# Kernel tuning notes

Measured on AMD Instinct MI355X. Metric: run time of the kernel, lower is better.

## Reference

```python
import jax, jax.numpy as jnp
import numpy as np

SR = 16000
FLOOR = 60.0
EPS = 1e-12

# ---------- numpy helpers replicating the torch control flow (plan building) ----------

def _hann(n):
    # torch.hann_window default periodic=True: 0.5 - 0.5*cos(2*pi*k/n)
    if n <= 0:
        return np.zeros((0,), np.float32)
    return (0.5 - 0.5 * np.cos(2.0 * np.pi * np.arange(n) / n)).astype(np.float32)


def _interp_linear(p, T):
    # torch F.interpolate(mode='linear', align_corners=False) on [1,1,S] -> [1,1,T]
    S = p.shape[0]
    pos = (np.arange(T, dtype=np.float64) + 0.5) * (S / T) - 0.5
    pos = np.clip(pos, 0.0, S - 1)
    lo = np.floor(pos).astype(np.int64)
    hi = np.minimum(lo + 1, S - 1)
    frac = pos - lo
    return (p[lo] * (1.0 - frac) + p[hi] * frac).astype(np.float32)


def _find_voiced(f0, i):
    sub = f0[i:]
    if sub.size == 0:
        return None
    flag = (sub > 0.0).astype(np.int64)
    flag[0] = 0
    if not flag.any():
        return None
    idx = int(flag.argmax())
    rest = flag[idx:]
    z = np.nonzero(rest == 0)[0]
    cnt = int(z[0]) if z.size else int(rest.size)
    left = i + idx
    return left, left + cnt


def _find_allpeaks(sig, f0, sr, floor=FLOOR):
    T = sig.shape[0]
    gpeak = float(np.abs(sig).max())

    def find_peak(i, dir_):
        w = int(sr / max(float(f0[i]), floor))
        s = max(i - w // 2, 0)
        if dir_ == 'left':
            cl, cr = max(int(i - 1.75 * w), 0), max(int(i - 1.3 * w), 0)
        else:
            cl, cr = int(i + 0.3 * w), int(i + 0.75 * w)
        if cl == cr or T - cl < w or s + w > T:
            return w, -1.0, i, 0.0
        seg = np.lib.stride_tricks.sliding_window_view(sig[cl:min(T, cr + w)], w)
        segn = seg / np.maximum(np.linalg.norm(seg, axis=-1, keepdims=True), EPS)
        tmpl = sig[s:s + w]
        tmpl = tmpl / max(float(np.linalg.norm(tmpl)), EPS)
        corr = segn @ tmpl
        r = int(corr.argmax())
        return w, float(corr[r]), i + (r + cl) - s, float(np.abs(seg[r]).max())

    added_right, i, peaks = -1e308, 0, []
    while True:
        v = _find_voiced(f0, i)
        if v is None:
            break
        left, right = v
        middle = (left + right) // 2
        w = int(sr / float(f0[middle]))
        s = max(middle - w // 2, 0)
        win = sig[s:s + w]
        mn, imn = float(win.min()), int(win.argmin())
        mx, imx = float(win.max()), int(win.argmax())
        if mn == mx:
            i = middle
        else:
            i = s + (imn if abs(mn) > abs(mx) else imx)
        backup = i
        while True:
            w, corr, i, peak = find_peak(i, 'left')
            if corr == -1.0:
                i -= w
            if i < left:
                if corr > 0.7 and peak > 0.023333 * gpeak and i - added_right > 0.8 * w:
                    peaks.append(i)
                break
            if corr > 0.3 and (peak == 0.0 or peak > 0.01 * gpeak):
                if i - added_right > 0.8 * w:
                    peaks.append(i)
        i = backup
        while True:
            w, corr, i, peak = find_peak(i, 'right')
            if corr == -1.0:
                i += w
            if i >= right:
                if corr > 0.7 and peak > 0.023333 * gpeak:
                    peaks.append(i)
                    added_right = i
                break
            if corr > 0.3 and (peak == 0.0 or peak > 0.01 * gpeak):
                peaks.append(i)
                added_right = i
        i = right
    if not peaks:
        return None
    return np.clip(np.sort(np.array(peaks, np.int64)), 0, T - 1)


def _psola_plan(T, f0, peaks, sr, floor=FLOOR):
    # Returns (dst_idx, src_idx, wgt, tail_i) s.t.
    #   new = zeros; new[dst] += wgt * x[src]; new[tail_i:] = x[tail_i:]
    max_w = 1.25 * sr / float(f0[f0 > 0].min())
    dsts, srcs, ws = [], [], []

    def add_op(dst0, src0, win):
        n = win.shape[0]
        if n > 0:
            dsts.append(dst0 + np.arange(n, dtype=np.int64))
            srcs.append(src0 + np.arange(n, dtype=np.int64))
            ws.append(win)

    i = 0
    while i < T:
        v = _find_voiced(f0, i)
        if v is None:
            break
        left_v, right_v = v
        add_op(i, i, _hann(left_v - i))  # hann fade over unvoiced gap
        while left_v < right_v:
            p = int(np.abs(peaks - left_v).argmin())
            period = int(sr / max(float(f0[left_v]), floor))
            lw = rw = period // 2
            if p > 0 and peaks[p] - peaks[p - 1] <= max_w:
                lw = min(int(peaks[p] - peaks[p - 1]), lw)
            if p < len(peaks) - 1 and peaks[p + 1] - peaks[p] <= max_w:
                rw = min(int(peaks[p + 1] - peaks[p]), rw)
            li = max(int(peaks[p]) - lw, 0)
            ri = int(peaks[p]) + rw
            ival = (ri - li) // 2
            if ival <= 0:  # safety guard vs duplicate peaks (torch code would stall)
                left_v += max(period, 1)
                continue
            win = _hann(2 * ival)
            a, b = left_v - ival, left_v + ival
            st, sp, _ = slice(a, b).indices(T)        # python/torch slice semantics
            dst_len = max(0, sp - st)
            src_len = max(0, min(T, li + 2 * ival) - li)
            seglen = min(dst_len, src_len)
            st2, _, _ = slice(a, a + seglen).indices(T)
            add_op(st2, li, win[:seglen])
            left_v += ival * 2
        i = right_v
    if dsts:
        dst = np.concatenate(dsts)
        src = np.concatenate(srcs)
        wgt = np.concatenate(ws)
    else:
        dst = np.zeros((0,), np.int64)
        src = np.zeros((0,), np.int64)
        wgt = np.zeros((0,), np.float32)
    return dst, src, wgt, min(i, T)


def build_plan(snd_np, pitch_np, pitch_shift, pitch_range):
    T = snd_np.shape[0]
    x = snd_np - snd_np.mean()
    f0 = _interp_linear(pitch_np, T)
    peaks = _find_allpeaks(x, f0, SR)
    assert peaks is not None, 'no peaks found'
    voiced = np.sort(f0[f0 > 0.0])
    median = float(voiced[(voiced.size - 1) // 2]) * pitch_shift  # torch median = lower middle
    f0 = f0 * pitch_shift
    f0 = np.where(f0 > 0.0, median + (f0 - median) * pitch_range, 0.0)
    return _psola_plan(T, f0, peaks, SR)


# ---------- harness entry points ----------

def setup_inputs() -> dict:
    key = jax.random.key(0)
    k1, k2 = jax.random.split(key)
    T = 3_840_000   # 240 s at 16 kHz
    S = 15_000      # pitch frames (hop 256)
    t = jnp.arange(T, dtype=jnp.float32) / SR
    # pitched signal + noise so peak correlation thresholds fire like real speech
    snd = 0.5 * jnp.sin(2.0 * jnp.pi * 130.0 * t) + 0.05 * jax.random.normal(k1, (T,), jnp.float32)
    base = 100.0 + 80.0 * jax.random.uniform(k2, (S,), jnp.float32)
    voiced = ((jnp.arange(S) // 250) % 5) != 4   # voiced runs with unvoiced gaps
    pitch = jnp.where(voiced, base, 0.0)
    return {'snd': snd, 'pitch': pitch, 'pitch_shift': 1.2, 'pitch_range': 0.8}


def reference(snd, pitch, pitch_shift, pitch_range):
    snd_np = np.asarray(snd, np.float32)
    pitch_np = np.asarray(pitch, np.float32)
    dst, src, wgt, tail = build_plan(snd_np, pitch_np, float(pitch_shift), float(pitch_range))
    dst_j = jnp.asarray(dst)
    src_j = jnp.asarray(src)
    wgt_j = jnp.asarray(wgt)
    x = snd - jnp.mean(snd)
    out = jnp.zeros_like(x).at[dst_j].add(wgt_j * x[src_j])
    # final unvoiced tail is a SET (overwrites any OLA spill), matching torch order
    mask = jnp.arange(x.shape[0]) >= tail
    return jnp.where(mask, x, out)
```

## Files before the change

kernel.cpp:

```cpp
#include <hip/hip_runtime.h>
#include <math.h>
#include <limits.h>

typedef long long ll;

#define MAXCHAIN 4096
#define MAXP 49152
#define MAXOPS 49152
#define MAXR 64
#define PART_OFF 4096
#define CHAINS_OFF 16384
#define PEAKS_OFF (CHAINS_OFF + 128 * MAXCHAIN * 4)
#define OPS_OFF (PEAKS_OFF + MAXP * 4)
#define F0_OFF (OPS_OFF + (size_t)MAXOPS * 16)

static __device__ const double TWOPI = 6.283185307179586;

struct Ctrl {
  double gpeak, max_w, ps64;
  long long k_rem, tail;
  float mean32, median_raw, md32, minv_scaled32;
  unsigned amax_bits, minf0_bits, prefix;
  int cnt_pos, shift, n_starts, n_ends, nregions, n_peaks, n_ops;
  int hist[256];
  int region_start[MAXR], region_end[MAXR];
  int chain_cnt[128];
  int chain_off[129];
};

__device__ __forceinline__ double dmul(double a, double b) { return __dmul_rn(a, b); }
__device__ __forceinline__ double dadd(double a, double b) { return __dadd_rn(a, b); }
__device__ __forceinline__ double dsub(double a, double b) { return __dadd_rn(a, -b); }
__device__ __forceinline__ float fmul(float a, float b) { return __fmul_rn(a, b); }
__device__ __forceinline__ float fadd(float a, float b) { return __fadd_rn(a, b); }
__device__ __forceinline__ float fsub(float a, float b) { return __fadd_rn(a, -b); }

__device__ __forceinline__ float xval(const float* snd, float mean, ll t) {
  return fsub(snd[t], mean);
}

__device__ __forceinline__ float div_exact(float x, float d, float r) {
  float q = __fmul_rn(x, r);
  float e = __fmaf_rn(-d, q, x);
  return __fmaf_rn(e, r, q);
}

__device__ float f0_at(const float* pitch, ll t, ll S, double ratio) {
  double pos = dsub(dmul(dadd((double)t, 0.5), ratio), 0.5);
  double hi = (double)(S - 1);
  pos = fmin(fmax(pos, 0.0), hi);
  double fl = floor(pos);
  ll lo = (ll)fl;
  if (lo < 0) lo = 0;
  if (lo > S - 1) lo = S - 1;
  ll hii = lo + 1; if (hii > S - 1) hii = S - 1;
  double frac = dsub(pos, fl);
  double om = dsub(1.0, frac);
  double v = dadd(dmul((double)pitch[lo], om), dmul((double)pitch[hii], frac));
  return (float)v;
}

__device__ float pw_blk_l(const float* __restrict__ buf, int base, int n, float& pk) {
  if (n < 8) {
    float res = 0.0f;
    for (int i = 0; i < n; ++i) {
      float x = buf[base + i];
      pk = fmaxf(pk, fabsf(x));
      res = fadd(res, fmul(x, x));
    }
    return res;
  }
  float x0 = buf[base + 0], x1 = buf[base + 1], x2 = buf[base + 2], x3 = buf[base + 3],
        x4 = buf[base + 4], x5 = buf[base + 5], x6 = buf[base + 6], x7 = buf[base + 7];
  pk = fmaxf(pk, fabsf(x0)); pk = fmaxf(pk, fabsf(x1));
  pk = fmaxf(pk, fabsf(x2)); pk = fmaxf(pk, fabsf(x3));
  pk = fmaxf(pk, fabsf(x4)); pk = fmaxf(pk, fabsf(x5));
  pk = fmaxf(pk, fabsf(x6)); pk = fmaxf(pk, fabsf(x7));
  float r0 = fmul(x0, x0), r1 = fmul(x1, x1), r2 = fmul(x2, x2), r3 = fmul(x3, x3);
  float r4 = fmul(x4, x4), r5 = fmul(x5, x5), r6 = fmul(x6, x6), r7 = fmul(x7, x7);
  int i = 8, lim = n - (n & 7);
  for (; i < lim; i += 8) {
    float y;
    y = buf[base + i + 0]; pk = fmaxf(pk, fabsf(y)); r0 = fadd(r0, fmul(y, y));
    y = buf[base + i + 1]; pk = fmaxf(pk, fabsf(y)); r1 = fadd(r1, fmul(y, y));
    y = buf[base + i + 2]; pk = fmaxf(pk, fabsf(y)); r2 = fadd(r2, fmul(y, y));
    y = buf[base + i + 3]; pk = fmaxf(pk, fabsf(y)); r3 = fadd(r3, fmul(y, y));
    y = buf[base + i + 4]; pk = fmaxf(pk, fabsf(y)); r4 = fadd(r4, fmul(y, y));
    y = buf[base + i + 5]; pk = fmaxf(pk, fabsf(y)); r5 = fadd(r5, fmul(y, y));
    y = buf[base + i + 6]; pk = fmaxf(pk, fabsf(y)); r6 = fadd(r6, fmul(y, y));
    y = buf[base + i + 7]; pk = fmaxf(pk, fabsf(y)); r7 = fadd(r7, fmul(y, y));
  }
  float res = fadd(fadd(fadd(r0, r1), fadd(r2, r3)), fadd(fadd(r4, r5), fadd(r6, r7)));
  for (; i < n; ++i) {
    float y = buf[base + i];
    pk = fmaxf(pk, fabsf(y));
    res = fadd(res, fmul(y, y));
  }
  return res;
}

__device__ float pw_sq_pk_l(const float* __restrict__ buf, int base, int n, float& pk) {
  if (n <= 128) return pw_blk_l(buf, base, n, pk);
  int n2 = (n >> 1); n2 -= (n2 & 7);
  float a = pw_blk_l(buf, base, n2, pk);
  int m = n - n2;
  float b;
  if (m <= 128) {
    b = pw_blk_l(buf, base + n2, m, pk);
  } else {
    int m2 = (m >> 1); m2 -= (m2 & 7);
    float b1 = pw_blk_l(buf, base + n2, m2, pk);
    float b2 = pw_blk_l(buf, base + n2 + m2, m - m2, pk);
    b = fadd(b1, b2);
  }
  return fadd(a, b);
}

__device__ float dot_lds(const float* __restrict__ buf, int base, float d, float r,
                         const float* __restrict__ tm, int w) {
  float a0 = 0.f, a1 = 0.f, a2 = 0.f, a3 = 0.f, a4 = 0.f, a5 = 0.f, a6 = 0.f, a7 = 0.f;
  int lim = w - (w & 7);
  int k = 0;
  for (; k < lim; k += 8) {
    a0 = __fmaf_rn(div_exact(buf[base + k + 0], d, r), tm[k + 0], a0);
    a1 = __fmaf_rn(div_exact(buf[base + k + 1], d, r), tm[k + 1], a1);
    a2 = __fmaf_rn(div_exact(buf[base + k + 2], d, r), tm[k + 2], a2);
    a3 = __fmaf_rn(div_exact(buf[base + k + 3], d, r), tm[k + 3], a3);
    a4 = __fmaf_rn(div_exact(buf[base + k + 4], d, r), tm[k + 4], a4);
    a5 = __fmaf_rn(div_exact(buf[base + k + 5], d, r), tm[k + 5], a5);
    a6 = __fmaf_rn(div_exact(buf[base + k + 6], d, r), tm[k + 6], a6);
    a7 = __fmaf_rn(div_exact(buf[base + k + 7], d, r), tm[k + 7], a7);
  }
  if (k + 0 < w) a0 = __fmaf_rn(div_exact(buf[base + k + 0], d, r), tm[k + 0], a0);
  if (k + 1 < w) a1 = __fmaf_rn(div_exact(buf[base + k + 1], d, r), tm[k + 1], a1);
  if (k + 2 < w) a2 = __fmaf_rn(div_exact(buf[base + k + 2], d, r), tm[k + 2], a2);
  if (k + 3 < w) a3 = __fmaf_rn(div_exact(buf[base + k + 3], d, r), tm[k + 3], a3);
  if (k + 4 < w) a4 = __fmaf_rn(div_exact(buf[base + k + 4], d, r), tm[k + 4], a4);
  if (k + 5 < w) a5 = __fmaf_rn(div_exact(buf[base + k + 5], d, r), tm[k + 5], a5);
  if (k + 6 < w) a6 = __fmaf_rn(div_exact(buf[base + k + 6], d, r), tm[k + 6], a6);
  return fadd(fadd(fadd(a0, a1), fadd(a2, a3)), fadd(fadd(a4, a5), fadd(a6, a7)));
}

__global__ void k_init(char* wsb) {
  Ctrl* c = (Ctrl*)wsb;
  int t = threadIdx.x;
  for (int b = t; b < 256; b += blockDim.x) c->hist[b] = 0;
  for (int b = t; b < 128; b += blockDim.x) c->chain_cnt[b] = 0;
  if (t == 0) {
    c->amax_bits = 0u; c->minf0_bits = 0xFFFFFFFFu;
    c->cnt_pos = 0; c->n_starts = 0; c->n_ends = 0; c->n_ops = 0;
    c->nregions = 0; c->n_peaks = 0; c->tail = 0;
  }
}

__global__ void k_sum_partial(const float* __restrict__ snd, ll T, char* wsb) {
  __shared__ double sd[256];
  double local = 0.0;
  ll stride = (ll)gridDim.x * blockDim.x;
  for (ll t = (ll)blockIdx.x * blockDim.x + threadIdx.x; t < T; t += stride)
    local += (double)snd[t];
  sd[threadIdx.x] = local; __syncthreads();
  for (int o = 128; o > 0; o >>= 1) {
    if ((int)threadIdx.x < o) sd[threadIdx.x] += sd[threadIdx.x + o];
    __syncthreads();
  }
  if (threadIdx.x == 0) ((double*)(wsb + PART_OFF))[blockIdx.x] = sd[0];
}

__global__ void k_sum_final(char* wsb, ll T, int nparts) {
  __shared__ double sd[256];
  double local = 0.0;
  const double* p = (const double*)(wsb + PART_OFF);
  for (int i = threadIdx.x; i < nparts; i += blockDim.x) local += p[i];
  sd[threadIdx.x] = local; __syncthreads();
  for (int o = 128; o > 0; o >>= 1) {
    if ((int)threadIdx.x < o) sd[threadIdx.x] += sd[threadIdx.x + o];
    __syncthreads();
  }
  if (threadIdx.x == 0) ((Ctrl*)wsb)->mean32 = (float)(sd[0] / (double)T);
}

__global__ void k_f0(const float* __restrict__ pitch, ll T, ll S, double ratio,
                     unsigned* __restrict__ bits) {
  ll stride = (ll)gridDim.x * blockDim.x;
  for (ll t = (ll)blockIdx.x * blockDim.x + threadIdx.x; t < T; t += stride)
    bits[t] = __float_as_uint(f0_at(pitch, t, S, ratio));
}

__global__ void k_scan(const float* __restrict__ snd, const float* __restrict__ pitch,
                       ll T, ll S, double ratio, char* wsb,
                       const unsigned* __restrict__ f0bits, int cached) {
  Ctrl* c = (Ctrl*)wsb;
  float mean = c->mean32;
  __shared__ unsigned smax[256]; __shared__ unsigned smin[256]; __shared__ int scnt[256];
  unsigned mymax = 0u, mymin = 0xFFFFFFFFu; int mycnt = 0;
  ll stride = (ll)gridDim.x * blockDim.x;
  for (ll t = (ll)blockIdx.x * blockDim.x + threadIdx.x; t < T; t += stride) {
    float xv = xval(snd, mean, t);
    unsigned ab = __float_as_uint(fabsf(xv));
    if (ab > mymax) mymax = ab;
    float f = cached ? __uint_as_float(f0bits[t]) : f0_at(pitch, t, S, ratio);
    bool pos = (f > 0.0f);
    if (pos) { ++mycnt; unsigned fb = __float_as_uint(f); if (fb < mymin) mymin = fb; }
    if (t >= 1) {
      float fp = cached ? __uint_as_float(f0bits[t - 1]) : f0_at(pitch, t - 1, S, ratio);
      bool posp = (fp > 0.0f);
      if (pos && (t == 1 || !posp)) {
        int id = atomicAdd(&c->n_starts, 1);
        if (id < MAXR) c->region_start[id] = (int)t;
      }
      if (!pos && posp && (t - 1) >= 1) {
        int id = atomicAdd(&c->n_ends, 1);
        if (id < MAXR) c->region_end[id] = (int)t;
      }
    }
    if (t == T - 1 && pos) {
      int id = atomicAdd(&c->n_ends, 1);
      if (id < MAXR) c->region_end[id] = (int)T;
    }
  }
  smax[threadIdx.x] = mymax; smin[threadIdx.x] = mymin; scnt[threadIdx.x] = mycnt;
  __syncthreads();
  for (int o = 128; o > 0; o >>= 1) {
    if ((int)threadIdx.x < o) {
      if (smax[threadIdx.x + o] > smax[threadIdx.x]) smax[threadIdx.x] = smax[threadIdx.x + o];
      if (smin[threadIdx.x + o] < smin[threadIdx.x]) smin[threadIdx.x] = smin[threadIdx.x + o];
      scnt[threadIdx.x] += scnt[threadIdx.x + o];
    }
    __syncthreads();
  }
  if (threadIdx.x == 0) {
    atomicMax(&c->amax_bits, smax[0]);
    atomicMin(&c->minf0_bits, smin[0]);
    atomicAdd(&c->cnt_pos, scnt[0]);
  }
}

__global__ void k_prep(char* wsb, const float* ps) {
  Ctrl* c = (Ctrl*)wsb;
  int ns = c->n_starts; if (ns > MAXR) ns = MAXR;
  int ne = c->n_ends; if (ne > MAXR) ne = MAXR;
  for (int a = 1; a < ns; ++a) {
    int v = c->region_start[a]; int b = a - 1;
    while (b >= 0 && c->region_start[b] > v) { c->region_start[b + 1] = c->region_start[b]; --b; }
    c->region_start[b + 1] = v;
  }
  for (int a = 1; a < ne; ++a) {
    int v = c->region_end[a]; int b = a - 1;
    while (b >= 0 && c->region_end[b] > v) { c->region_end[b + 1] = c->region_end[b]; --b; }
    c->region_end[b + 1] = v;
  }
  int nr = ns < ne ? ns : ne;
  c->nregions = nr;
  c->tail = (nr > 0) ? (ll)c->region_end[nr - 1] : 0;
  c->gpeak = (double)__uint_as_float(c->amax_bits);
  ll cnt = (ll)c->cnt_pos; if (cnt < 1) cnt = 1;
  c->k_rem = (cnt - 1) / 2;
  c->prefix = 0u; c->shift = 24;
  double p64 = (double)ps[0];
  c->ps64 = round(p64 * 1e7) / 1e7;
}

__global__ void k_hist(const float* __restrict__ pitch, ll T, ll S, double ratio, char* wsb,
                       const unsigned* __restrict__ f0bits, int cached) {
  Ctrl* c = (Ctrl*)wsb;
  __shared__ int h[256];
  for (int b = threadIdx.x; b < 256; b += blockDim.x) h[b] = 0;
  __syncthreads();
  int shift = c->shift;
  unsigned pref = c->prefix;
  unsigned himask = (shift == 24) ? 0u : ((~0u) << (shift + 8));
  ll stride = (ll)gridDim.x * blockDim.x;
  for (ll t = (ll)blockIdx.x * blockDim.x + threadIdx.x; t < T; t += stride) {
    float f; unsigned bits;
    if (cached) { bits = f0bits[t]; f = __uint_as_float(bits); }
    else { f = f0_at(pitch, t, S, ratio); bits = __float_as_uint(f); }
    if (f > 0.0f) {
      if ((bits & himask) == (pref & himask)) atomicAdd(&h[(bits >> shift) & 255], 1);
    }
  }
  __syncthreads();
  for (int b = threadIdx.x; b < 256; b += blockDim.x) if (h[b]) atomicAdd(&c->hist[b], h[b]);
}

__global__ void k_sel(char* wsb, const float* ps, const float* pr) {
  Ctrl* c = (Ctrl*)wsb;
  int shift = c->shift;
  ll k = c->k_rem;
  ll run = 0; int pick = 255;
  for (int b = 0; b < 256; ++b) {
    ll h = (ll)c->hist[b];
    if (run + h > k) { pick = b; break; }
    run += h;
  }
  c->prefix |= ((unsigned)pick) << shift;
  c->k_rem = k - run;
  for (int b = 0; b < 256; ++b) c->hist[b] = 0;
  if (shift == 0) {
    float mraw = __uint_as_float(c->prefix);
    c->median_raw = mraw;
    double md = dmul((double)mraw, c->ps64);
    float md32 = (float)md;
    c->md32 = md32;
    float minf = __uint_as_float(c->minf0_bits);
    float u = fmul(minf, ps[0]);
    float sc = fadd(md32, fmul(fsub(u, md32), pr[0]));
    c->minv_scaled32 = sc;
    c->max_w = 20000.0 / (double)sc;
  }
  c->shift = shift - 8;
}

#define WALK_MAXI 400000

__global__ __launch_bounds__(64) void k_walks(const float* __restrict__ snd,
                                              const float* __restrict__ pitch,
                                              ll T, ll S, double ratio, char* wsb,
                                              const unsigned* __restrict__ f0bits, int cached) {
  Ctrl* c = (Ctrl*)wsb;
  int chain = blockIdx.x;
  int reg = chain >> 1, dir = chain & 1;
  if (reg >= c->nregions) return;
  int* mybuf = ((int*)(wsb + CHAINS_OFF)) + (ll)chain * MAXCHAIN;
  ll left = (ll)c->region_start[reg];
  ll right = (ll)c->region_end[reg];
  float mean = c->mean32;
  double gpeak = c->gpeak;
  int lane = threadIdx.x;

  __shared__ float lx[608];
  __shared__ float ltm[272];

  ll i;
  {
    ll middle = (left + right) / 2;
    float f0m = cached ? __uint_as_float(f0bits[middle]) : f0_at(pitch, middle, S, ratio);
    int w0 = (int)(16000.0 / (double)f0m);
    ll s0 = middle - (ll)(w0 / 2); if (s0 < 0) s0 = 0;
    ll len = T - s0; if (len > (ll)w0) len = (ll)w0;
    float mn = 0.f, mx = 0.f; ll imn = 0, imx = 0; bool first = true;
    for (ll k = 0; k < len; ++k) {
      float v = xval(snd, mean, s0 + k);
      if (first) { mn = mx = v; imn = imx = 0; first = false; }
      else {
        if (v < mn) { mn = v; imn = k; }
        if (v > mx) { mx = v; imx = k; }
      }
    }
    if (mn == mx) i = middle;
    else i = s0 + ((fabs((double)mn) > fabs((double)mx)) ? imn : imx);
  }

  double added_right = -1e308;
  int cnt = 0;
  bool stop = false;

  for (int iter = 0; iter < WALK_MAXI && !stop; ++iter) {
    float f0v = cached ? __uint_as_float(f0bits[i]) : f0_at(pitch, i, S, ratio);
    int w = (int)(16000.0 / fmax((double)f0v, 60.0));
    ll cl, cr;
    if (dir == 0) {
      cl = (ll)dsub((double)i, dmul(1.75, (double)w)); if (cl < 0) cl = 0;
      cr = (ll)dsub((double)i, dmul(1.3, (double)w)); if (cr < 0) cr = 0;
    } else {
      cl = (ll)dadd((double)i, dmul(0.3, (double)w));
      cr = (ll)dadd((double)i, dmul(0.75, (double)w));
    }
    ll s = i - (ll)(w / 2); if (s < 0) s = 0;
    bool valid = !(cl == cr || (T - cl) < (ll)w || (s + (ll)w) > T);
    double corrd; ll ipos; double peakd;
    if (!valid) { corrd = -1.0; ipos = i; peakd = 0.0; }
    else {
      ll L = cr + (ll)w; if (L > T) L = T; L -= cl;
      int ncand = (int)(L - (ll)w + 1);
      ll lo = (s < cl) ? s : cl;
      ll hiA = s + (ll)w;
      ll hiB = cl + L;
      ll hi = (hiA > hiB) ? hiA : hiB;
      int len = (int)(hi - lo);
      __syncthreads();
      for (int k = lane; k < len; k += 64) lx[k] = fsub(snd[lo + k], mean);
      __syncthreads();
      int toff = (int)(s - lo);
      int coff = (int)(cl - lo);
      float dummy = 0.0f;
      float tn = __fsqrt_rn(pw_sq_pk_l(lx, toff, w, dummy));
      float tdiv = (float)fmax((double)tn, 1e-12);
      float rt = __fdiv_rn(1.0f, tdiv);
      for (int k = lane; k < w; k += 64) ltm[k] = div_exact(lx[toff + k], tdiv, rt);
      __syncthreads();
      int r0 = lane;
      int rc0 = (r0 < ncand) ? r0 : (ncand - 1);
      float pk0 = 0.0f;
      float nr0 = __fsqrt_rn(pw_sq_pk_l(lx, coff + rc0, w, pk0));
      float divr0 = fmaxf(nr0, (float)1e-12);
      float rr0 = __fdiv_rn(1.0f, divr0);
      float co0 = dot_lds(lx, coff + rc0, divr0, rr0, ltm, w);
      float pk1 = 0.0f, co1 = -INFINITY;
      if (ncand > 64) {
        int r1 = lane + 64;
        int rc1 = (r1 < ncand) ? r1 : (ncand - 1);
        float nr1 = __fsqrt_rn(pw_sq_pk_l(lx, coff + rc1, w, pk1));
        float divr1 = fmaxf(nr1, (float)1e-12);
        float rr1 = __fdiv_rn(1.0f, divr1);
        co1 = dot_lds(lx, coff + rc1, divr1, rr1, ltm, w);
        if (r1 >= ncand) co1 = -INFINITY;
      }
      float bv = (r0 < ncand) ? co0 : -INFINITY;
      int bi = (r0 < ncand) ? r0 : 0x7FFFFFFF;
      {
        int i1 = lane + 64;
        if (co1 > bv || (co1 == bv && i1 < bi)) { bv = co1; bi = i1; }
      }
      for (int off = 32; off > 0; off >>= 1) {
        float ov = __shfl_xor(bv, off);
        int oi = __shfl_xor(bi, off);
        if (ov > bv || (ov == bv && oi < bi)) { bv = ov; bi = oi; }
      }
      corrd = (double)bv;
      ipos = i + ((ll)bi + cl) - s;
      {
        int ol = bi & 63;
        float p0 = __shfl(pk0, ol);
        float p1 = __shfl(pk1, ol);
        peakd = (double)((bi < 64) ? p0 : p1);
      }
    }
    ll inew;
    if (dir == 0) {
      inew = (corrd == -1.0) ? (i - (ll)w) : ipos;
      if (inew < left) {
        if (corrd > 0.7 && peakd > dmul(0.023333, gpeak) &&
            (dsub((double)inew, added_right) > dmul(0.8, (double)w))) {
          if (cnt < MAXCHAIN) { if (lane == 0) mybuf[cnt] = (int)inew; ++cnt; }
        }
        stop = true;
      } else {
        if (corrd > 0.3 && (peakd == 0.0 || peakd > dmul(0.01, gpeak))) {
          if (dsub((double)inew, added_right) > dmul(0.8, (double)w)) {
            if (cnt < MAXCHAIN) { if (lane == 0) mybuf[cnt] = (int)inew; ++cnt; }
          }
        }
        i = inew;
      }
    } else {
      inew = (corrd == -1.0) ? (i + (ll)w) : ipos;
      if (inew >= right) {
        if (corrd > 0.7 && peakd > dmul(0.023333, gpeak)) {
          if (cnt < MAXCHAIN) { if (lane == 0) mybuf[cnt] = (int)inew; ++cnt; }
        }
        stop = true;
      } else {
        if (corrd > 0.3 && (peakd == 0.0 || peakd > dmul(0.01, gpeak))) {
          if (cnt < MAXCHAIN) { if (lane == 0) mybuf[cnt] = (int)inew; ++cnt; }
          added_right = (double)inew;
        }
        i = inew;
      }
    }
  }
  if (lane == 0) c->chain_cnt[chain] = cnt;
}

__global__ void k_offsets(char* wsb) {
  Ctrl* c = (Ctrl*)wsb;
  int off = 0;
  for (int ch = 0; ch < 128; ++ch) {
    c->chain_off[ch] = off;
    off += c->chain_cnt[ch];
  }
  c->chain_off[128] = off;
  c->n_peaks = (off > MAXP) ? MAXP : off;
}

__global__ void k_gather(char* wsb, ll T) {
  Ctrl* c = (Ctrl*)wsb;
  int chain = blockIdx.x;
  int cnt = c->chain_cnt[chain];
  int off = c->chain_off[chain];
  const int* mybuf = ((const int*)(wsb + CHAINS_OFF)) + (ll)chain * MAXCHAIN;
  int* peaks = (int*)(wsb + PEAKS_OFF);
  int dir = chain & 1;
  for (int k = threadIdx.x; k < cnt; k += blockDim.x) {
    if (off + k < MAXP) {
      int v = dir ? mybuf[k] : mybuf[cnt - 1 - k];
      if (v < 0) v = 0;
      if ((ll)v > T - 1) v = (int)(T - 1);
      peaks[off + k] = v;
    }
  }
}

#define PSLDS 3584

__global__ __launch_bounds__(64) void k_psola(const float* __restrict__ pitch, ll T, ll S,
                                              double ratio, char* wsb,
                                              const float* ps, const float* pr,
                                              const unsigned* __restrict__ f0bits, int cached) {
  Ctrl* c = (Ctrl*)wsb;
  int r = blockIdx.x;
  if (r >= c->nregions) return;
  const int* peaks = (const int*)(wsb + PEAKS_OFF);
  int np = c->n_peaks;
  int tid = threadIdx.x;
  ll left = (ll)c->region_start[r], right = (ll)c->region_end[r];

  __shared__ int lp[PSLDS];
  __shared__ int sh_g0, sh_g1, sh_use;

  if (np > 0) {
    if (tid == 0) {
      int lo = 0, hi = np;
      ll tgt = left - 512;
      while (lo < hi) { int m = (lo + hi) >> 1; if ((ll)peaks[m] < tgt) lo = m + 1; else hi = m; }
      int a = lo;
      lo = 0; hi = np; tgt = right + 512;
      while (lo < hi) { int m = (lo + hi) >> 1; if ((ll)peaks[m] < tgt) lo = m + 1; else hi = m; }
      int b = lo;
      a -= 4; if (a < 0) a = 0;
      b += 4; if (b > np) b = np;
      sh_g0 = a; sh_g1 = b; sh_use = (b - a <= PSLDS) ? 1 : 0;
    }
    __syncthreads();
    if (sh_use) {
      for (int k = sh_g0 + tid; k < sh_g1; k += 64) lp[k - sh_g0] = peaks[k];
    }
    __syncthreads();
  }
  if (tid != 0) return;

  int g0 = (np > 0 && sh_use) ? sh_g0 : 0;
  const int* pk = (np > 0 && sh_use) ? lp : peaks;

  int4* ops = (int4*)(wsb + OPS_OFF);
  ll prev_end = (r == 0) ? 0 : (ll)c->region_end[r - 1];
  ll lv = left, rv = right;
  double max_w = c->max_w;
  float md32 = c->md32, psv = ps[0], prv = pr[0];

  ll gapn = lv - prev_end;
  if (gapn > 0) {
    int o = atomicAdd(&c->n_ops, 1);
    if (o < MAXOPS) ops[o] = make_int4((int)prev_end, (int)prev_end, (int)gapn, (int)gapn);
  }
  if (np <= 0) return;
  int j;
  {
    int loJ = 0, hiJ = np;
    while (loJ < hiJ) {
      int mid = (loJ + hiJ) >> 1;
      if ((ll)peaks[mid] < lv) loJ = mid + 1; else hiJ = mid;
    }
    j = loJ;
  }
  for (long itc = 0; itc < 2000000 && lv < rv; ++itc) {
    float f = cached ? __uint_as_float(f0bits[lv]) : f0_at(pitch, lv, S, ratio);
    float u = fmul(f, psv);
    float fs = (!(u > 0.0f)) ? 0.0f : fadd(md32, fmul(fsub(u, md32), prv));
    int period = (int)(16000.0 / fmax((double)fs, 60.0));
    int lw = period / 2, rw = period / 2;
    while (j < np && (ll)pk[j - g0] < lv) ++j;
    ll dl = (j > 0) ? (lv - (ll)pk[j - 1 - g0]) : LLONG_MAX;
    ll dr = (j < np) ? ((ll)pk[j - g0] - lv) : LLONG_MAX;
    int p;
    if (dl <= dr) {
      int q = j - 1; int v = pk[q - g0];
      while (q > 0 && pk[q - 1 - g0] == v) --q;
      p = q;
    } else {
      int q = j; int v = pk[q - g0];
      while (q > 0 && pk[q - 1 - g0] == v) --q;
      p = q;
    }
    if (p > 0) {
      ll g = (ll)pk[p - g0] - (ll)pk[p - 1 - g0];
      if ((double)g <= max_w && g < (ll)lw) lw = (int)g;
    }
    if (p < np - 1) {
      ll g = (ll)pk[p + 1 - g0] - (ll)pk[p - g0];
      if ((double)g <= max_w && g < (ll)rw) rw = (int)g;
    }
    ll li = (ll)pk[p - g0] - (ll)lw; if (li < 0) li = 0;
    ll ri = (ll)pk[p - g0] + (ll)rw;
    ll ival = (ri - li) / 2;
    if (ival <= 0) { lv += (period > 1 ? (ll)period : 1); continue; }
    ll a = lv - ival, b = lv + ival;
    ll st = (a < 0) ? ((a + T > 0) ? a + T : 0) : ((a < T) ? a : T);
    ll sp = (b < 0) ? ((b + T > 0) ? b + T : 0) : ((b < T) ? b : T);
    ll dst_len = sp - st; if (dst_len < 0) dst_len = 0;
    ll se = li + 2 * ival; if (se > T) se = T;
    ll src_len = se - li; if (src_len < 0) src_len = 0;
    ll seglen = dst_len < src_len ? dst_len : src_len;
    if (seglen > 0) {
      int o = atomicAdd(&c->n_ops, 1);
      if (o < MAXOPS) ops[o] = make_int4((int)st, (int)li, (int)seglen, (int)(2 * ival));
    }
    lv += 2 * ival;
  }
}

__global__ void k_scatter(const float* __restrict__ snd, char* wsb, float* out, ll T) {
  Ctrl* c = (Ctrl*)wsb;
  float mean = c->mean32;
  int nops = c->n_ops; if (nops > MAXOPS) nops = MAXOPS;
  const int4* ops = (const int4*)(wsb + OPS_OFF);
  for (int o = blockIdx.x; o < nops; o += gridDim.x) {
    int4 op = ops[o];
    ll dst = (ll)op.x, src = (ll)op.y; int n = op.z, m = op.w;
    for (int k = threadIdx.x; k < n; k += blockDim.x) {
      double ang = dmul(TWOPI, (double)k) / (double)m;
      float w32 = (float)dsub(0.5, dmul(0.5, cos(ang)));
      float val = fmul(w32, xval(snd, mean, src + k));
      atomicAdd(&out[dst + k], val);
    }
  }
}

__global__ void k_final(const float* __restrict__ snd, char* wsb, float* out, ll T) {
  Ctrl* c = (Ctrl*)wsb;
  float mean = c->mean32;
  ll tail = c->tail;
  ll stride = (ll)gridDim.x * blockDim.x;
  for (ll t = (ll)blockIdx.x * blockDim.x + threadIdx.x; t < T; t += stride)
    if (t >= tail) out[t] = xval(snd, mean, t);
}

extern "C" void kernel_launch(void* const* d_in, const int* in_sizes, int n_in,
                              void* d_out, int out_size, void* d_ws, size_t ws_size,
                              hipStream_t stream) {
  ll T = (ll)in_sizes[0];
  ll S = (ll)in_sizes[1];
  const float* snd = (const float*)d_in[0];
  const float* pitch = (const float*)d_in[1];
  const float* ps = (const float*)d_in[2];
  const float* pr = (const float*)d_in[3];
  float* out = (float*)d_out;
  char* wsb = (char*)d_ws;
  double ratio = (double)S / (double)T;

  size_t f0_need = F0_OFF + (size_t)T * 4;
  int cached = (ws_size >= f0_need) ? 1 : 0;
  unsigned* f0bits = (unsigned*)(wsb + F0_OFF);

  k_init<<<1, 256, 0, stream>>>(wsb);
  k_sum_partial<<<1024, 256, 0, stream>>>(snd, T, wsb);
  k_sum_final<<<1, 256, 0, stream>>>(wsb, T, 1024);
  if (cached) k_f0<<<2048, 256, 0, stream>>>(pitch, T, S, ratio, f0bits);
  k_scan<<<2048, 256, 0, stream>>>(snd, pitch, T, S, ratio, wsb, f0bits, cached);
  k_prep<<<1, 1, 0, stream>>>(wsb, ps);
  for (int pass = 0; pass < 4; ++pass) {
    k_hist<<<2048, 256, 0, stream>>>(pitch, T, S, ratio, wsb, f0bits, cached);
    k_sel<<<1, 1, 0, stream>>>(wsb, ps, pr);
  }
  k_walks<<<128, 64, 0, stream>>>(snd, pitch, T, S, ratio, wsb, f0bits, cached);
  k_offsets<<<1, 1, 0, stream>>>(wsb);
  k_gather<<<128, 64, 0, stream>>>(wsb, T);
  k_psola<<<64, 64, 0, stream>>>(pitch, T, S, ratio, wsb, ps, pr, f0bits, cached);
  hipMemsetAsync(d_out, 0, (size_t)out_size * sizeof(float), stream);
  k_scatter<<<8192, 128, 0, stream>>>(snd, wsb, out, T);
  k_final<<<2048, 256, 0, stream>>>(snd, wsb, out, T);
}
```

Before: 14.17 ms.

## Stage pitch frames in LDS for walks/psola, prefetch snd, per-region op slabs

The serial walk and PSOLA kernels now load the pitch frames covering their region into shared memory and interpolate f0 from there, instead of reading a global cached f0 array on every iteration. The walk kernel also preloads the snd window into registers before the barrier, which overlaps the global load latency. PSOLA writes its ops into fixed per-region slabs rather than through a global atomic counter, and the scatter kernel iterates over those slabs. The aim is to cut the global-memory latency on these latency-bound single-thread loops. The cost is slab capacity limits, since ops beyond a slab are dropped, and scatter blocks that skip empty slab entries.

New measurement: 13.61 ms. 1.04x faster.

```diff
diff --git a/kernel.cpp b/kernel.cpp
--- a/kernel.cpp
+++ b/kernel.cpp
@@ -21,11 +21,12 @@
   long long k_rem, tail;
   float mean32, median_raw, md32, minv_scaled32;
   unsigned amax_bits, minf0_bits, prefix;
-  int cnt_pos, shift, n_starts, n_ends, nregions, n_peaks, n_ops;
+  int cnt_pos, shift, n_starts, n_ends, nregions, n_peaks, n_ops, slab;
   int hist[256];
   int region_start[MAXR], region_end[MAXR];
   int chain_cnt[128];
   int chain_off[129];
+  int region_ops[MAXR];
 };
 
 __device__ __forceinline__ double dmul(double a, double b) { return __dmul_rn(a, b); }
@@ -58,6 +59,32 @@
   double om = dsub(1.0, frac);
   double v = dadd(dmul((double)pitch[lo], om), dmul((double)pitch[hii], frac));
   return (float)v;
+}
+
+__device__ __forceinline__ ll frame_lo(ll t, ll S, double ratio) {
+  double pos = dsub(dmul(dadd((double)t, 0.5), ratio), 0.5);
+  pos = fmin(fmax(pos, 0.0), (double)(S - 1));
+  ll lo = (ll)floor(pos);
+  if (lo < 0) lo = 0;
+  if (lo > S - 1) lo = S - 1;
+  return lo;
+}
+
+__device__ __forceinline__ float f0_lds(const float* __restrict__ lpitch, int p0, int p1,
+                                        const float* __restrict__ pitch,
+                                        ll t, ll S, double ratio) {
+  double pos = dsub(dmul(dadd((double)t, 0.5), ratio), 0.5);
+  pos = fmin(fmax(pos, 0.0), (double)(S - 1));
+  double fl = floor(pos);
+  ll lo = (ll)fl;
+  if (lo < 0) lo = 0;
+  if (lo > S - 1) lo = S - 1;
+  ll hii = lo + 1; if (hii > S - 1) hii = S - 1;
+  double frac = dsub(pos, fl);
+  double om = dsub(1.0, frac);
+  float plo = (lo >= p0 && lo <= p1) ? lpitch[(int)(lo - p0)] : pitch[lo];
+  float phi = (hii >= p0 && hii <= p1) ? lpitch[(int)(hii - p0)] : pitch[hii];
+  return (float)dadd(dmul((double)plo, om), dmul((double)phi, frac));
 }
 
 __device__ float pw_blk_l(const float* __restrict__ buf, int base, int n, float& pk) {
@@ -146,10 +173,11 @@
   int t = threadIdx.x;
   for (int b = t; b < 256; b += blockDim.x) c->hist[b] = 0;
   for (int b = t; b < 128; b += blockDim.x) c->chain_cnt[b] = 0;
+  for (int b = t; b < MAXR; b += blockDim.x) c->region_ops[b] = 0;
   if (t == 0) {
     c->amax_bits = 0u; c->minf0_bits = 0xFFFFFFFFu;
     c->cnt_pos = 0; c->n_starts = 0; c->n_ends = 0; c->n_ops = 0;
-    c->nregions = 0; c->n_peaks = 0; c->tail = 0;
+    c->nregions = 0; c->n_peaks = 0; c->tail = 0; c->slab = MAXOPS;
   }
 }
 
@@ -257,6 +285,7 @@
   ll cnt = (ll)c->cnt_pos; if (cnt < 1) cnt = 1;
   c->k_rem = (cnt - 1) / 2;
   c->prefix = 0u; c->shift = 24;
+  c->slab = MAXOPS / (nr > 0 ? nr : 1);
   double p64 = (double)ps[0];
   c->ps64 = round(p64 * 1e7) / 1e7;
 }
@@ -312,11 +341,11 @@
 }
 
 #define WALK_MAXI 400000
+#define WPS 1664
 
 __global__ __launch_bounds__(64) void k_walks(const float* __restrict__ snd,
                                               const float* __restrict__ pitch,
-                                              ll T, ll S, double ratio, char* wsb,
-                                              const unsigned* __restrict__ f0bits, int cached) {
+                                              ll T, ll S, double ratio, char* wsb) {
   Ctrl* c = (Ctrl*)wsb;
   int chain = blockIdx.x;
   int reg = chain >> 1, dir = chain & 1;
@@ -328,13 +357,26 @@
   double gpeak = c->gpeak;
   int lane = threadIdx.x;
 
-  __shared__ float lx[608];
+  __shared__ float lx[640];
   __shared__ float ltm[272];
+  __shared__ float lpitch[WPS];
+
+  ll tA = left - 600; if (tA < 0) tA = 0;
+  ll tB = right + 600; if (tB > T - 1) tB = T - 1;
+  ll p0l = frame_lo(tA, S, ratio);
+  ll p1l = frame_lo(tB, S, ratio) + 1; if (p1l > S - 1) p1l = S - 1;
+  int p0 = (int)p0l, p1 = (int)p1l;
+  int span = p1 - p0 + 1;
+  bool puse = (span <= WPS);
+  if (puse) {
+    for (int k = lane; k < span; k += 64) lpitch[k] = pitch[p0 + k];
+  } else { p0 = 0; p1 = -1; }
+  __syncthreads();
 
   ll i;
   {
     ll middle = (left + right) / 2;
-    float f0m = cached ? __uint_as_float(f0bits[middle]) : f0_at(pitch, middle, S, ratio);
+    float f0m = f0_lds(lpitch, p0, p1, pitch, middle, S, ratio);
     int w0 = (int)(16000.0 / (double)f0m);
     ll s0 = middle - (ll)(w0 / 2); if (s0 < 0) s0 = 0;
     ll len = T - s0; if (len > (ll)w0) len = (ll)w0;
@@ -356,7 +398,7 @@
   bool stop = false;
 
   for (int iter = 0; iter < WALK_MAXI && !stop; ++iter) {
-    float f0v = cached ? __uint_as_float(f0bits[i]) : f0_at(pitch, i, S, ratio);
+    float f0v = f0_lds(lpitch, p0, p1, pitch, i, S, ratio);
     int w = (int)(16000.0 / fmax((double)f0v, 60.0));
     ll cl, cr;
     if (dir == 0) {
@@ -378,8 +420,19 @@
       ll hiB = cl + L;
       ll hi = (hiA > hiB) ? hiA : hiB;
       int len = (int)(hi - lo);
+      float stg[10];
+      #pragma unroll
+      for (int j = 0; j < 10; ++j) {
+        ll a = lo + (ll)(j * 64) + lane;
+        if (a > T - 1) a = T - 1;
+        stg[j] = snd[a];
+      }
       __syncthreads();
-      for (int k = lane; k < len; k += 64) lx[k] = fsub(snd[lo + k], mean);
+      #pragma unroll
+      for (int j = 0; j < 10; ++j) {
+        int k = j * 64 + lane;
+        if (k < len) lx[k] = fsub(stg[j], mean);
+      }
       __syncthreads();
       int toff = (int)(s - lo);
       int coff = (int)(cl - lo);
@@ -421,9 +474,9 @@
       ipos = i + ((ll)bi + cl) - s;
       {
         int ol = bi & 63;
-        float p0 = __shfl(pk0, ol);
-        float p1 = __shfl(pk1, ol);
-        peakd = (double)((bi < 64) ? p0 : p1);
+        float p0f = __shfl(pk0, ol);
+        float p1f = __shfl(pk1, ol);
+        peakd = (double)((bi < 64) ? p0f : p1f);
       }
     }
     ll inew;
@@ -492,11 +545,11 @@
 }
 
 #define PSLDS 3584
+#define PPS 2048
 
 __global__ __launch_bounds__(64) void k_psola(const float* __restrict__ pitch, ll T, ll S,
                                               double ratio, char* wsb,
-                                              const float* ps, const float* pr,
-                                              const unsigned* __restrict__ f0bits, int cached) {
+                                              const float* ps, const float* pr) {
   Ctrl* c = (Ctrl*)wsb;
   int r = blockIdx.x;
   if (r >= c->nregions) return;
@@ -506,7 +559,18 @@
   ll left = (ll)c->region_start[r], right = (ll)c->region_end[r];
 
   __shared__ int lp[PSLDS];
+  __shared__ float lpitch[PPS];
   __shared__ int sh_g0, sh_g1, sh_use;
+
+  ll tA = left - 600; if (tA < 0) tA = 0;
+  ll tB = right + 600; if (tB > T - 1) tB = T - 1;
+  ll p0l = frame_lo(tA, S, ratio);
+  ll p1l = frame_lo(tB, S, ratio) + 1; if (p1l > S - 1) p1l = S - 1;
+  int p0 = (int)p0l, p1 = (int)p1l;
+  int span = p1 - p0 + 1;
+  if (span <= PPS) {
+    for (int k = tid; k < span; k += 64) lpitch[k] = pitch[p0 + k];
+  } else { p0 = 0; p1 = -1; }
 
   if (np > 0) {
     if (tid == 0) {
@@ -525,14 +589,16 @@
     if (sh_use) {
       for (int k = sh_g0 + tid; k < sh_g1; k += 64) lp[k - sh_g0] = peaks[k];
     }
-    __syncthreads();
-  }
+  }
+  __syncthreads();
   if (tid != 0) return;
 
   int g0 = (np > 0 && sh_use) ? sh_g0 : 0;
   const int* pk = (np > 0 && sh_use) ? lp : peaks;
 
-  int4* ops = (int4*)(wsb + OPS_OFF);
+  int slab = c->slab;
+  int4* myops = ((int4*)(wsb + OPS_OFF)) + (ll)r * slab;
+  int cnt = 0;
   ll prev_end = (r == 0) ? 0 : (ll)c->region_end[r - 1];
   ll lv = left, rv = right;
   double max_w = c->max_w;
@@ -540,72 +606,79 @@
 
   ll gapn = lv - prev_end;
   if (gapn > 0) {
-    int o = atomicAdd(&c->n_ops, 1);
-    if (o < MAXOPS) ops[o] = make_int4((int)prev_end, (int)prev_end, (int)gapn, (int)gapn);
-  }
-  if (np <= 0) return;
-  int j;
-  {
-    int loJ = 0, hiJ = np;
-    while (loJ < hiJ) {
-      int mid = (loJ + hiJ) >> 1;
-      if ((ll)peaks[mid] < lv) loJ = mid + 1; else hiJ = mid;
-    }
-    j = loJ;
-  }
-  for (long itc = 0; itc < 2000000 && lv < rv; ++itc) {
-    float f = cached ? __uint_as_float(f0bits[lv]) : f0_at(pitch, lv, S, ratio);
-    float u = fmul(f, psv);
-    float fs = (!(u > 0.0f)) ? 0.0f : fadd(md32, fmul(fsub(u, md32), prv));
-    int period = (int)(16000.0 / fmax((double)fs, 60.0));
-    int lw = period / 2, rw = period / 2;
-    while (j < np && (ll)pk[j - g0] < lv) ++j;
-    ll dl = (j > 0) ? (lv - (ll)pk[j - 1 - g0]) : LLONG_MAX;
-    ll dr = (j < np) ? ((ll)pk[j - g0] - lv) : LLONG_MAX;
-    int p;
-    if (dl <= dr) {
-      int q = j - 1; int v = pk[q - g0];
-      while (q > 0 && pk[q - 1 - g0] == v) --q;
-      p = q;
-    } else {
-      int q = j; int v = pk[q - g0];
-      while (q > 0 && pk[q - 1 - g0] == v) --q;
-      p = q;
-    }
-    if (p > 0) {
-      ll g = (ll)pk[p - g0] - (ll)pk[p - 1 - g0];
-      if ((double)g <= max_w && g < (ll)lw) lw = (int)g;
-    }
-    if (p < np - 1) {
-      ll g = (ll)pk[p + 1 - g0] - (ll)pk[p - g0];
-      if ((double)g <= max_w && g < (ll)rw) rw = (int)g;
-    }
-    ll li = (ll)pk[p - g0] - (ll)lw; if (li < 0) li = 0;
-    ll ri = (ll)pk[p - g0] + (ll)rw;
-    ll ival = (ri - li) / 2;
-    if (ival <= 0) { lv += (period > 1 ? (ll)period : 1); continue; }
-    ll a = lv - ival, b = lv + ival;
-    ll st = (a < 0) ? ((a + T > 0) ? a + T : 0) : ((a < T) ? a : T);
-    ll sp = (b < 0) ? ((b + T > 0) ? b + T : 0) : ((b < T) ? b : T);
-    ll dst_len = sp - st; if (dst_len < 0) dst_len = 0;
-    ll se = li + 2 * ival; if (se > T) se = T;
-    ll src_len = se - li; if (src_len < 0) src_len = 0;
-    ll seglen = dst_len < src_len ? dst_len : src_len;
-    if (seglen > 0) {
-      int o = atomicAdd(&c->n_ops, 1);
-      if (o < MAXOPS) ops[o] = make_int4((int)st, (int)li, (int)seglen, (int)(2 * ival));
-    }
-    lv += 2 * ival;
-  }
+    if (cnt < slab) myops[cnt] = make_int4((int)prev_end, (int)prev_end, (int)gapn, (int)gapn);
+    ++cnt;
+  }
+  if (np > 0) {
+    int j;
+    {
+      int loJ = 0, hiJ = np;
+      while (loJ < hiJ) {
+        int mid = (loJ + hiJ) >> 1;
+        if ((ll)peaks[mid] < lv) loJ = mid + 1; else hiJ = mid;
+      }
+      j = loJ;
+    }
+    for (long itc = 0; itc < 2000000 && lv < rv; ++itc) {
+      float f = f0_lds(lpitch, p0, p1, pitch, lv, S, ratio);
+      float u = fmul(f, psv);
+      float fs = (!(u > 0.0f)) ? 0.0f : fadd(md32, fmul(fsub(u, md32), prv));
+      int period = (int)(16000.0 / fmax((double)fs, 60.0));
+      int lw = period / 2, rw = period / 2;
+      while (j < np && (ll)pk[j - g0] < lv) ++j;
+      ll dl = (j > 0) ? (lv - (ll)pk[j - 1 - g0]) : LLONG_MAX;
+      ll dr = (j < np) ? ((ll)pk[j - g0] - lv) : LLONG_MAX;
+      int p;
+      if (dl <= dr) {
+        int q = j - 1; int v = pk[q - g0];
+        while (q > 0 && pk[q - 1 - g0] == v) --q;
+        p = q;
+      } else {
+        int q = j; int v = pk[q - g0];
+        while (q > 0 && pk[q - 1 - g0] == v) --q;
+        p = q;
+      }
+      if (p > 0) {
+        ll g = (ll)pk[p - g0] - (ll)pk[p - 1 - g0];
+        if ((double)g <= max_w && g < (ll)lw) lw = (int)g;
+      }
+      if (p < np - 1) {
+        ll g = (ll)pk[p + 1 - g0] - (ll)pk[p - g0];
+        if ((double)g <= max_w && g < (ll)rw) rw = (int)g;
+      }
+      ll li = (ll)pk[p - g0] - (ll)lw; if (li < 0) li = 0;
+      ll ri = (ll)pk[p - g0] + (ll)rw;
+      ll ival = (ri - li) / 2;
+      if (ival <= 0) { lv += (period > 1 ? (ll)period : 1); continue; }
+      ll a = lv - ival, b = lv + ival;
+      ll st = (a < 0) ? ((a + T > 0) ? a + T : 0) : ((a < T) ? a : T);
+      ll sp = (b < 0) ? ((b + T > 0) ? b + T : 0) : ((b < T) ? b : T);
+      ll dst_len = sp - st; if (dst_len < 0) dst_len = 0;
+      ll se = li + 2 * ival; if (se > T) se = T;
+      ll src_len = se - li; if (src_len < 0) src_len = 0;
+      ll seglen = dst_len < src_len ? dst_len : src_len;
+      if (seglen > 0) {
+        if (cnt < slab) myops[cnt] = make_int4((int)st, (int)li, (int)seglen, (int)(2 * ival));
+        ++cnt;
+      }
+      lv += 2 * ival;
+    }
+  }
+  c->region_ops[r] = (cnt > slab) ? slab : cnt;
 }
 
 __global__ void k_scatter(const float* __restrict__ snd, char* wsb, float* out, ll T) {
   Ctrl* c = (Ctrl*)wsb;
   float mean = c->mean32;
-  int nops = c->n_ops; if (nops > MAXOPS) nops = MAXOPS;
+  int nr = c->nregions; if (nr > MAXR) nr = MAXR;
+  int slab = c->slab;
   const int4* ops = (const int4*)(wsb + OPS_OFF);
-  for (int o = blockIdx.x; o < nops; o += gridDim.x) {
-    int4 op = ops[o];
+  ll total = (ll)nr * slab;
+  for (ll idx = blockIdx.x; idx < total; idx += gridDim.x) {
+    int r = (int)(idx / slab);
+    int o = (int)(idx - (ll)r * slab);
+    if (o >= c->region_ops[r]) continue;
+    int4 op = ops[(ll)r * slab + o];
     ll dst = (ll)op.x, src = (ll)op.y; int n = op.z, m = op.w;
     for (int k = threadIdx.x; k < n; k += blockDim.x) {
       double ang = dmul(TWOPI, (double)k) / (double)m;
@@ -652,10 +725,10 @@
     k_hist<<<2048, 256, 0, stream>>>(pitch, T, S, ratio, wsb, f0bits, cached);
     k_sel<<<1, 1, 0, stream>>>(wsb, ps, pr);
   }
-  k_walks<<<128, 64, 0, stream>>>(snd, pitch, T, S, ratio, wsb, f0bits, cached);
+  k_walks<<<128, 64, 0, stream>>>(snd, pitch, T, S, ratio, wsb);
   k_offsets<<<1, 1, 0, stream>>>(wsb);
   k_gather<<<128, 64, 0, stream>>>(wsb, T);
-  k_psola<<<64, 64, 0, stream>>>(pitch, T, S, ratio, wsb, ps, pr, f0bits, cached);
+  k_psola<<<64, 64, 0, stream>>>(pitch, T, S, ratio, wsb, ps, pr);
   hipMemsetAsync(d_out, 0, (size_t)out_size * sizeof(float), stream);
   k_scatter<<<8192, 128, 0, stream>>>(snd, wsb, out, T);
   k_final<<<2048, 256, 0, stream>>>(snd, wsb, out, T);
```
